# Kernel tuning notes

Measured on AMD Instinct MI355X. Metric: run time of the kernel, lower is better.

The kernel has to match this reference:

```python
import jax, jax.numpy as jnp
import numpy as np

N_EMB = 1024
N_HEADS = 16


def setup_inputs() -> dict:
    key = jax.random.key(0)
    k1, k2, k3 = jax.random.split(key, 3)
    x = jax.random.normal(k1, (2, 2048, N_EMB), dtype=jnp.float32)
    # qkv linear params (torch Linear: y = x @ W.T + b; store W as [in, 3*in])
    W_qkv = jax.random.normal(k2, (N_EMB, 3 * N_EMB), dtype=jnp.float32) * (1.0 / np.sqrt(N_EMB))
    b_qkv = jax.random.normal(k3, (3 * N_EMB,), dtype=jnp.float32) * 0.02
    return {"x": x, "W_qkv": W_qkv, "b_qkv": b_qkv}


def reference(x, W_qkv, b_qkv):
    B, S, D = x.shape
    H = N_HEADS
    Dh = D // H
    qkv = x @ W_qkv + b_qkv                       # [B, S, 3D]
    q, k, v = jnp.split(qkv, 3, axis=-1)
    # [B, S, D] -> [B, H, S, Dh]
    q = q.reshape(B, S, H, Dh).transpose(0, 2, 1, 3)
    k = k.reshape(B, S, H, Dh).transpose(0, 2, 1, 3)
    v = v.reshape(B, S, H, Dh).transpose(0, 2, 1, 3)
    scores = jnp.einsum("bhqd,bhkd->bhqk", q, k) * (1.0 / np.sqrt(Dh))
    attn = jax.nn.softmax(scores, axis=-1)        # no causal mask in original
    out = jnp.einsum("bhqk,bhkd->bhqd", attn, v)  # [B, H, S, Dh]
    return out.transpose(0, 2, 1, 3).reshape(B, S, D)
```

## Files before the change

### kernel.cpp

```cpp
#include <hip/hip_runtime.h>

#define S_LEN 2048
#define D_EMB 1024
#define H_CNT 16
#define DHD   64
#define N_QKV 3072

typedef __attribute__((ext_vector_type(8))) short short8;
typedef __attribute__((ext_vector_type(4))) float f32x4;
typedef __attribute__((ext_vector_type(4))) unsigned u32x4;
typedef unsigned short u16;

__device__ __forceinline__ u16 f2bf(float f) {
  unsigned u = __float_as_uint(f);
  u += 0x7FFFu + ((u >> 16) & 1u);
  return (u16)(u >> 16);
}

__device__ __forceinline__ unsigned cvtpk(float lo, float hi) {
  unsigned r;
  asm("v_cvt_pk_bf16_f32 %0, %1, %2" : "=v"(r) : "v"(lo), "v"(hi));
  return r;
}

__device__ __forceinline__ void gload16(const void* g, void* lds) {
  __builtin_amdgcn_global_load_lds(
      (const __attribute__((address_space(1))) void*)g,
      (__attribute__((address_space(3))) void*)lds, 16, 0, 0);
}

__global__ __launch_bounds__(256) void cvt_x_kern(const float* __restrict__ x,
                                                  u16* __restrict__ xb) {
  int i = blockIdx.x * 256 + threadIdx.x;
  float4 v = ((const float4*)x)[i];
  unsigned* o = (unsigned*)&((ushort4*)xb)[i];
  o[0] = cvtpk(v.x, v.y);
  o[1] = cvtpk(v.z, v.w);
}

__global__ __launch_bounds__(256) void cvt_wt_kern(const float* __restrict__ w,
                                                   u16* __restrict__ wt) {
  __shared__ u16 tile[64][65];
  const int ct = blockIdx.x, kt = blockIdx.y, t = threadIdx.x;
#pragma unroll
  for (int i = 0; i < 4; ++i) {
    int idx = t + i * 256;
    int kk = idx >> 4, c4 = (idx & 15) * 4;
    float4 v = *(const float4*)(w + (size_t)(kt * 64 + kk) * N_QKV + ct * 64 + c4);
    tile[kk][c4 + 0] = f2bf(v.x);
    tile[kk][c4 + 1] = f2bf(v.y);
    tile[kk][c4 + 2] = f2bf(v.z);
    tile[kk][c4 + 3] = f2bf(v.w);
  }
  __syncthreads();
#pragma unroll
  for (int i = 0; i < 2; ++i) {
    int id = t + i * 256;
    int c = id >> 3, k8 = (id & 7) * 8;
    short8 o;
#pragma unroll
    for (int j = 0; j < 8; ++j) o[j] = (short)tile[k8 + j][c];
    *(short8*)&wt[(size_t)(ct * 64 + c) * D_EMB + kt * 64 + k8] = o;
  }
}

__global__ __launch_bounds__(256) void qkv_gemm_kern(
    const u16* __restrict__ xb, const u16* __restrict__ wt,
    const float* __restrict__ bias,
    u16* __restrict__ qo, u16* __restrict__ ko, u16* __restrict__ vo) {
  __shared__ __align__(16) u16 SM[128 * 128];
  u16* As = SM;
  u16* Bs = SM + 128 * 64;
  const int t = threadIdx.x;
  const int w = t >> 6, l = t & 63, lr = l & 15, lg = l >> 4;
  const int wr = w >> 1, wc = w & 1;
  const int row0 = blockIdx.x * 128, col0 = blockIdx.y * 128;
  const int srow = l >> 3, scol = (l & 7) * 16;
  const int tsel = col0 >> 10;
  const bool ctq = (tsel < 2);

  f32x4 acc[4][4];
#pragma unroll
  for (int m = 0; m < 4; ++m)
#pragma unroll
    for (int n = 0; n < 4; ++n) acc[m][n] = (f32x4){0.f, 0.f, 0.f, 0.f};

  const int ldrow = w * 32;
  for (int ki = 0; ki < 16; ++ki) {
    int k0 = ki * 64;
#pragma unroll
    for (int c = 0; c < 4; ++c) {
      int tr = ldrow + c * 8 + srow;
      int sc = scol ^ ((tr & 7) << 4);
      gload16((const char*)xb + (size_t)(row0 + tr) * (D_EMB * 2) + k0 * 2 + sc,
              (char*)As + (ldrow + c * 8) * 128);
      gload16((const char*)wt + (size_t)(col0 + tr) * (D_EMB * 2) + k0 * 2 + sc,
              (char*)Bs + (ldrow + c * 8) * 128);
    }
    __syncthreads();
    const u16* Ab = ctq ? Bs : As;
    const u16* Bb = ctq ? As : Bs;
    const int ar0 = ctq ? wc * 64 : wr * 64;
    const int br0 = ctq ? wr * 64 : wc * 64;
    short8 bfr[4][2];
#pragma unroll
    for (int n = 0; n < 4; ++n) {
      int br = br0 + n * 16 + lr;
#pragma unroll
      for (int kk = 0; kk < 2; ++kk)
        bfr[n][kk] = *(const short8*)&Bb[(br << 6) + ((kk * 32 + lg * 8) ^ ((br & 7) << 3))];
    }
#pragma unroll
    for (int m = 0; m < 4; ++m) {
      int ar = ar0 + m * 16 + lr;
      short8 a0 = *(const short8*)&Ab[(ar << 6) + ((lg * 8) ^ ((ar & 7) << 3))];
      short8 a1 = *(const short8*)&Ab[(ar << 6) + ((32 + lg * 8) ^ ((ar & 7) << 3))];
#pragma unroll
      for (int n = 0; n < 4; ++n) {
        acc[m][n] = __builtin_amdgcn_mfma_f32_16x16x32_bf16(a0, bfr[n][0], acc[m][n], 0, 0, 0);
        acc[m][n] = __builtin_amdgcn_mfma_f32_16x16x32_bf16(a1, bfr[n][1], acc[m][n], 0, 0, 0);
      }
    }
    __syncthreads();
  }

  const int bb = row0 >> 11;
  if (ctq) {
    const float scl = (tsel == 0) ? (0.125f * 1.44269504f) : 1.0f;
    u16* dst = (tsel == 0) ? qo : ko;
#pragma unroll
    for (int m = 0; m < 4; ++m) {
      int qc0 = wc * 64 + m * 16 + lg * 4;
      float4 bn = *(const float4*)&bias[col0 + qc0];
#pragma unroll
      for (int n = 0; n < 4; ++n) {
        int s = wr * 64 + n * 16 + lr;
        uint2 pk;
        pk.x = cvtpk((acc[m][n][0] + bn.x) * scl, (acc[m][n][1] + bn.y) * scl);
        pk.y = cvtpk((acc[m][n][2] + bn.z) * scl, (acc[m][n][3] + bn.w) * scl);
        *(uint2*)&SM[(s << 7) + (qc0 ^ ((s & 7) << 3))] = pk;
      }
    }
    __syncthreads();
    const int c = t & 15, rl = t >> 4;
#pragma unroll
    for (int pass = 0; pass < 8; ++pass) {
      int s = pass * 16 + rl;
      short8 v = *(const short8*)&SM[(s << 7) + ((c ^ (s & 7)) << 3)];
      int d = (col0 + c * 8) & 1023, hh = d >> 6, dh = d & 63;
      *(short8*)(dst + ((size_t)(bb * H_CNT + hh) * S_LEN + (row0 & 2047) + s) * DHD + dh) = v;
    }
  } else {
#pragma unroll
    for (int n = 0; n < 4; ++n) {
      int qc = wc * 64 + n * 16 + lr;
      float bn = bias[col0 + qc];
#pragma unroll
      for (int m = 0; m < 4; ++m) {
        int s0l = wr * 64 + m * 16 + lg * 4;
        uint2 pk;
        pk.x = cvtpk(acc[m][n][0] + bn, acc[m][n][1] + bn);
        pk.y = cvtpk(acc[m][n][2] + bn, acc[m][n][3] + bn);
        *(uint2*)&SM[(qc << 7) + (s0l ^ ((qc & 7) << 3))] = pk;
      }
    }
    __syncthreads();
    const int c = t & 15, rl = t >> 4;
#pragma unroll
    for (int pass = 0; pass < 8; ++pass) {
      int qc = pass * 16 + rl;
      short8 v = *(const short8*)&SM[(qc << 7) + ((c ^ (qc & 7)) << 3)];
      int d = (col0 + qc) & 1023, hh = d >> 6, dh = d & 63;
      *(short8*)(vo + ((size_t)(bb * H_CNT + hh) * DHD + dh) * S_LEN +
                 (row0 & 2047) + c * 8) = v;
    }
  }
}

__global__ __launch_bounds__(256) void attn_kern(
    const u16* __restrict__ qp, const u16* __restrict__ kp,
    const u16* __restrict__ vtp, float* __restrict__ out) {
  __shared__ __align__(16) u16 Ks[2][64 * 64];
  __shared__ __align__(16) u16 Vs[2][64 * 64];
  const int t = threadIdx.x;
  const int w = t >> 6, l = t & 63, lr = l & 15, lg = l >> 4;
  const int qt = blockIdx.x, bh = blockIdx.y;
  const int b = bh >> 4, h = bh & 15;
  const int srow = l >> 3, scol = (l & 7) * 16;

  const u16* qbase = qp + ((size_t)bh * S_LEN + qt * 64 + w * 16) * DHD;
  short8 qf[2];
#pragma unroll
  for (int kk = 0; kk < 2; ++kk)
    qf[kk] = *(const short8*)(qbase + lr * DHD + kk * 32 + lg * 8);

  float mrun = -__builtin_inff(), lsum = 0.f;
  f32x4 oacc[4];
#pragma unroll
  for (int ct = 0; ct < 4; ++ct) oacc[ct] = (f32x4){0.f, 0.f, 0.f, 0.f};

  const int lbase0 = lr * 64 + ((lg * 8) ^ ((lr & 7) << 3));
  const int lbase1 = lr * 64 + ((32 + lg * 8) ^ ((lr & 7) << 3));
  const u16* kb00 = &Ks[0][lbase0];
  const u16* kb01 = &Ks[0][lbase1];
  const u16* kb10 = &Ks[1][lbase0];
  const u16* kb11 = &Ks[1][lbase1];
  const u16* vb00 = &Vs[0][lbase0];
  const u16* vb01 = &Vs[0][lbase1];
  const u16* vb10 = &Vs[1][lbase0];
  const u16* vb11 = &Vs[1][lbase1];

  int koff[2], voff[2];
#pragma unroll
  for (int c = 0; c < 2; ++c) {
    int row = w * 16 + c * 8 + srow;
    int sc = scol ^ ((row & 7) << 4);
    int tau = ((row & 15) >> 2) * 8 + ((row >> 4) & 1) * 4 + (row & 3) + (row >> 5) * 32;
    koff[c] = tau * 128 + sc;
    voff[c] = row * (S_LEN * 2) + sc;
  }
  const char* kpt = (const char*)(kp + (size_t)bh * S_LEN * DHD);
  const char* vpt = (const char*)(vtp + (size_t)bh * DHD * S_LEN);

#define ATTN_STAGE(BUF)                                                   \
  {                                                                       \
    _Pragma("unroll") for (int c = 0; c < 2; ++c) {                       \
      int r8 = w * 16 + c * 8;                                            \
      gload16(kpt + koff[c], (char*)Ks[BUF] + r8 * 128);                  \
      gload16(vpt + voff[c], (char*)Vs[BUF] + r8 * 128);                  \
    }                                                                     \
    kpt += 64 * 128;                                                      \
    vpt += 64 * 2;                                                        \
  }

#define ATTN_TILE(KB0, KB1, VB0, VB1, PF, PBUF)                                   \
  {                                                                               \
    if (PF) ATTN_STAGE(PBUF)                                                      \
    f32x4 st[4];                                                                  \
    _Pragma("unroll") for (int k2 = 0; k2 < 4; ++k2)                              \
        st[k2] = (f32x4){0.f, 0.f, 0.f, 0.f};                                     \
    __builtin_amdgcn_s_setprio(1);                                                \
    _Pragma("unroll") for (int k2 = 0; k2 < 4; ++k2) {                            \
      short8 a0 = *(const short8*)(KB0 + k2 * 1024);                              \
      short8 a1 = *(const short8*)(KB1 + k2 * 1024);                              \
      st[k2] = __builtin_amdgcn_mfma_f32_16x16x32_bf16(a0, qf[0], st[k2], 0, 0, 0); \
      st[k2] = __builtin_amdgcn_mfma_f32_16x16x32_bf16(a1, qf[1], st[k2], 0, 0, 0); \
    }                                                                             \
    __builtin_amdgcn_s_setprio(0);                                                \
    float mx = fmaxf(fmaxf(fmaxf(st[0][0], st[0][1]), fmaxf(st[0][2], st[0][3])), \
                     fmaxf(fmaxf(st[1][0], st[1][1]), fmaxf(st[1][2], st[1][3]))); \
    mx = fmaxf(mx, fmaxf(fmaxf(fmaxf(st[2][0], st[2][1]), fmaxf(st[2][2], st[2][3])), \
                         fmaxf(fmaxf(st[3][0], st[3][1]), fmaxf(st[3][2], st[3][3])))); \
    mx = fmaxf(mx, __shfl_xor(mx, 16, 64));                                       \
    mx = fmaxf(mx, __shfl_xor(mx, 32, 64));                                       \
    if (!__all(mx - mrun <= 8.0f)) {                                              \
      float mnew = fmaxf(mrun, mx);                                               \
      float fsc = exp2f(mrun - mnew);                                             \
      float fr[4];                                                                \
      _Pragma("unroll") for (int r = 0; r < 4; ++r)                               \
          fr[r] = __shfl(fsc, lg * 4 + r, 64);                                    \
      _Pragma("unroll") for (int ct = 0; ct < 4; ++ct)                            \
        _Pragma("unroll") for (int r = 0; r < 4; ++r) oacc[ct][r] *= fr[r];       \
      lsum *= fsc;                                                                \
      mrun = mnew;                                                                \
    }                                                                             \
    float rs = 0.f;                                                               \
    _Pragma("unroll") for (int k2 = 0; k2 < 4; ++k2)                              \
      _Pragma("unroll") for (int r = 0; r < 4; ++r) {                             \
        st[k2][r] = exp2f(st[k2][r] - mrun);                                      \
        rs += st[k2][r];                                                          \
      }                                                                           \
    rs += __shfl_xor(rs, 16, 64);                                                 \
    rs += __shfl_xor(rs, 32, 64);                                                 \
    lsum += rs;                                                                   \
    u32x4 ua, ub;                                                                 \
    ua[0] = cvtpk(st[0][0], st[0][1]); ua[1] = cvtpk(st[0][2], st[0][3]);         \
    ua[2] = cvtpk(st[1][0], st[1][1]); ua[3] = cvtpk(st[1][2], st[1][3]);         \
    ub[0] = cvtpk(st[2][0], st[2][1]); ub[1] = cvtpk(st[2][2], st[2][3]);         \
    ub[2] = cvtpk(st[3][0], st[3][1]); ub[3] = cvtpk(st[3][2], st[3][3]);         \
    short8 pa0 = __builtin_bit_cast(short8, ua);                                  \
    short8 pa1 = __builtin_bit_cast(short8, ub);                                  \
    __builtin_amdgcn_s_setprio(1);                                                \
    _Pragma("unroll") for (int ct = 0; ct < 4; ++ct) {                            \
      short8 bv0 = *(const short8*)(VB0 + ct * 1024);                             \
      short8 bv1 = *(const short8*)(VB1 + ct * 1024);                             \
      oacc[ct] = __builtin_amdgcn_mfma_f32_16x16x32_bf16(pa0, bv0, oacc[ct], 0, 0, 0); \
      oacc[ct] = __builtin_amdgcn_mfma_f32_16x16x32_bf16(pa1, bv1, oacc[ct], 0, 0, 0); \
    }                                                                             \
    __builtin_amdgcn_s_setprio(0);                                                \
    __syncthreads();                                                              \
  }

  ATTN_STAGE(0)
  __syncthreads();
  for (int ii = 0; ii < 16; ++ii) {
    ATTN_TILE(kb00, kb01, vb00, vb01, 1, 1)
    ATTN_TILE(kb10, kb11, vb10, vb11, ii < 15, 0)
  }

  float inv = 1.0f / lsum;
  float invr[4];
#pragma unroll
  for (int r = 0; r < 4; ++r) invr[r] = __shfl(inv, lg * 4 + r, 64);
  const int qg0 = qt * 64 + w * 16 + lg * 4;
#pragma unroll
  for (int ct = 0; ct < 4; ++ct) {
    int col = h * 64 + ct * 16 + lr;
#pragma unroll
    for (int r = 0; r < 4; ++r)
      out[((size_t)b * S_LEN + qg0 + r) * D_EMB + col] = oacc[ct][r] * invr[r];
  }
}

extern "C" void kernel_launch(void* const* d_in, const int* in_sizes, int n_in,
                              void* d_out, int out_size, void* d_ws, size_t ws_size,
                              hipStream_t stream) {
  (void)in_sizes; (void)n_in; (void)out_size; (void)ws_size;
  const float* x  = (const float*)d_in[0];
  const float* Wq = (const float*)d_in[1];
  const float* bq = (const float*)d_in[2];
  float* out = (float*)d_out;
  char* ws = (char*)d_ws;
  u16* xb = (u16*)(ws);
  u16* wt = (u16*)(ws + (size_t)8  * 1024 * 1024);
  u16* qb = (u16*)(ws + (size_t)14 * 1024 * 1024);
  u16* kb = (u16*)(ws + (size_t)22 * 1024 * 1024);
  u16* vb = (u16*)(ws + (size_t)30 * 1024 * 1024);

  cvt_x_kern <<<4096, 256, 0, stream>>>(x, xb);
  cvt_wt_kern<<<dim3(48, 16), 256, 0, stream>>>(Wq, wt);
  qkv_gemm_kern<<<dim3(32, 24), 256, 0, stream>>>(xb, wt, bq, qb, kb, vb);
  attn_kern  <<<dim3(32, 32), 256, 0, stream>>>(qb, kb, vb, out);
}
```

Before: 190.7 us.

## Process two 16-row query groups per wave in attention kernel

```diff
diff --git a/kernel.cpp b/kernel.cpp
--- a/kernel.cpp
+++ b/kernel.cpp
@@ -188,16 +188,21 @@
   const int b = bh >> 4, h = bh & 15;
   const int srow = l >> 3, scol = (l & 7) * 16;
 
-  const u16* qbase = qp + ((size_t)bh * S_LEN + qt * 64 + w * 16) * DHD;
-  short8 qf[2];
-#pragma unroll
-  for (int kk = 0; kk < 2; ++kk)
-    qf[kk] = *(const short8*)(qbase + lr * DHD + kk * 32 + lg * 8);
-
-  float mrun = -__builtin_inff(), lsum = 0.f;
-  f32x4 oacc[4];
-#pragma unroll
-  for (int ct = 0; ct < 4; ++ct) oacc[ct] = (f32x4){0.f, 0.f, 0.f, 0.f};
+  const u16* qbase = qp + ((size_t)bh * S_LEN + qt * 128 + w * 32) * DHD;
+  short8 qf00, qf01, qf10, qf11;
+  qf00 = *(const short8*)(qbase + lr * DHD + 0 * 32 + lg * 8);
+  qf01 = *(const short8*)(qbase + lr * DHD + 1 * 32 + lg * 8);
+  qf10 = *(const short8*)(qbase + (16 + lr) * DHD + 0 * 32 + lg * 8);
+  qf11 = *(const short8*)(qbase + (16 + lr) * DHD + 1 * 32 + lg * 8);
+
+  float mrun0 = -__builtin_inff(), lsum0 = 0.f;
+  float mrun1 = -__builtin_inff(), lsum1 = 0.f;
+  f32x4 oacc0[4], oacc1[4];
+#pragma unroll
+  for (int ct = 0; ct < 4; ++ct) {
+    oacc0[ct] = (f32x4){0.f, 0.f, 0.f, 0.f};
+    oacc1[ct] = (f32x4){0.f, 0.f, 0.f, 0.f};
+  }
 
   const int lbase0 = lr * 64 + ((lg * 8) ^ ((lr & 7) << 3));
   const int lbase1 = lr * 64 + ((32 + lg * 8) ^ ((lr & 7) << 3));
@@ -233,59 +238,72 @@
     vpt += 64 * 2;                                                        \
   }
 
+#define SOFTMAX_G(ST, MRUN, LSUM, OACC, PA0, PA1)                                 \
+  {                                                                               \
+    float mx = fmaxf(fmaxf(fmaxf(ST[0][0], ST[0][1]), fmaxf(ST[0][2], ST[0][3])), \
+                     fmaxf(fmaxf(ST[1][0], ST[1][1]), fmaxf(ST[1][2], ST[1][3]))); \
+    mx = fmaxf(mx, fmaxf(fmaxf(fmaxf(ST[2][0], ST[2][1]), fmaxf(ST[2][2], ST[2][3])), \
+                         fmaxf(fmaxf(ST[3][0], ST[3][1]), fmaxf(ST[3][2], ST[3][3])))); \
+    mx = fmaxf(mx, __shfl_xor(mx, 16, 64));                                       \
+    mx = fmaxf(mx, __shfl_xor(mx, 32, 64));                                       \
+    if (!__all(mx - MRUN <= 8.0f)) {                                              \
+      float mnew = fmaxf(MRUN, mx);                                               \
+      float fsc = exp2f(MRUN - mnew);                                             \
+      float fr[4];                                                                \
+      _Pragma("unroll") for (int r = 0; r < 4; ++r)                               \
+          fr[r] = __shfl(fsc, lg * 4 + r, 64);                                    \
+      _Pragma("unroll") for (int ct = 0; ct < 4; ++ct)                            \
+        _Pragma("unroll") for (int r = 0; r < 4; ++r) OACC[ct][r] *= fr[r];       \
+      LSUM *= fsc;                                                                \
+      MRUN = mnew;                                                                \
+    }                                                                             \
+    float rs = 0.f;                                                               \
+    _Pragma("unroll") for (int k2 = 0; k2 < 4; ++k2)                              \
+      _Pragma("unroll") for (int r = 0; r < 4; ++r) {                             \
+        ST[k2][r] = exp2f(ST[k2][r] - MRUN);                                      \
+        rs += ST[k2][r];                                                          \
+      }                                                                           \
+    rs += __shfl_xor(rs, 16, 64);                                                 \
+    rs += __shfl_xor(rs, 32, 64);                                                 \
+    LSUM += rs;                                                                   \
+    u32x4 ua, ub;                                                                 \
+    ua[0] = cvtpk(ST[0][0], ST[0][1]); ua[1] = cvtpk(ST[0][2], ST[0][3]);         \
+    ua[2] = cvtpk(ST[1][0], ST[1][1]); ua[3] = cvtpk(ST[1][2], ST[1][3]);         \
+    ub[0] = cvtpk(ST[2][0], ST[2][1]); ub[1] = cvtpk(ST[2][2], ST[2][3]);         \
+    ub[2] = cvtpk(ST[3][0], ST[3][1]); ub[3] = cvtpk(ST[3][2], ST[3][3]);         \
+    PA0 = __builtin_bit_cast(short8, ua);                                         \
+    PA1 = __builtin_bit_cast(short8, ub);                                         \
+  }
+
 #define ATTN_TILE(KB0, KB1, VB0, VB1, PF, PBUF)                                   \
   {                                                                               \
     if (PF) ATTN_STAGE(PBUF)                                                      \
-    f32x4 st[4];                                                                  \
-    _Pragma("unroll") for (int k2 = 0; k2 < 4; ++k2)                              \
-        st[k2] = (f32x4){0.f, 0.f, 0.f, 0.f};                                     \
+    f32x4 st0[4], st1[4];                                                         \
+    _Pragma("unroll") for (int k2 = 0; k2 < 4; ++k2) {                            \
+      st0[k2] = (f32x4){0.f, 0.f, 0.f, 0.f};                                      \
+      st1[k2] = (f32x4){0.f, 0.f, 0.f, 0.f};                                      \
+    }                                                                             \
     __builtin_amdgcn_s_setprio(1);                                                \
     _Pragma("unroll") for (int k2 = 0; k2 < 4; ++k2) {                            \
       short8 a0 = *(const short8*)(KB0 + k2 * 1024);                              \
       short8 a1 = *(const short8*)(KB1 + k2 * 1024);                              \
-      st[k2] = __builtin_amdgcn_mfma_f32_16x16x32_bf16(a0, qf[0], st[k2], 0, 0, 0); \
-      st[k2] = __builtin_amdgcn_mfma_f32_16x16x32_bf16(a1, qf[1], st[k2], 0, 0, 0); \
+      st0[k2] = __builtin_amdgcn_mfma_f32_16x16x32_bf16(a0, qf00, st0[k2], 0, 0, 0); \
+      st0[k2] = __builtin_amdgcn_mfma_f32_16x16x32_bf16(a1, qf01, st0[k2], 0, 0, 0); \
+      st1[k2] = __builtin_amdgcn_mfma_f32_16x16x32_bf16(a0, qf10, st1[k2], 0, 0, 0); \
+      st1[k2] = __builtin_amdgcn_mfma_f32_16x16x32_bf16(a1, qf11, st1[k2], 0, 0, 0); \
     }                                                                             \
     __builtin_amdgcn_s_setprio(0);                                                \
-    float mx = fmaxf(fmaxf(fmaxf(st[0][0], st[0][1]), fmaxf(st[0][2], st[0][3])), \
-                     fmaxf(fmaxf(st[1][0], st[1][1]), fmaxf(st[1][2], st[1][3]))); \
-    mx = fmaxf(mx, fmaxf(fmaxf(fmaxf(st[2][0], st[2][1]), fmaxf(st[2][2], st[2][3])), \
-                         fmaxf(fmaxf(st[3][0], st[3][1]), fmaxf(st[3][2], st[3][3])))); \
-    mx = fmaxf(mx, __shfl_xor(mx, 16, 64));                                       \
-    mx = fmaxf(mx, __shfl_xor(mx, 32, 64));                                       \
-    if (!__all(mx - mrun <= 8.0f)) {                                              \
-      float mnew = fmaxf(mrun, mx);                                               \
-      float fsc = exp2f(mrun - mnew);                                             \
-      float fr[4];                                                                \
-      _Pragma("unroll") for (int r = 0; r < 4; ++r)                               \
-          fr[r] = __shfl(fsc, lg * 4 + r, 64);                                    \
-      _Pragma("unroll") for (int ct = 0; ct < 4; ++ct)                            \
-        _Pragma("unroll") for (int r = 0; r < 4; ++r) oacc[ct][r] *= fr[r];       \
-      lsum *= fsc;                                                                \
-      mrun = mnew;                                                                \
-    }                                                                             \
-    float rs = 0.f;                                                               \
-    _Pragma("unroll") for (int k2 = 0; k2 < 4; ++k2)                              \
-      _Pragma("unroll") for (int r = 0; r < 4; ++r) {                             \
-        st[k2][r] = exp2f(st[k2][r] - mrun);                                      \
-        rs += st[k2][r];                                                          \
-      }                                                                           \
-    rs += __shfl_xor(rs, 16, 64);                                                 \
-    rs += __shfl_xor(rs, 32, 64);                                                 \
-    lsum += rs;                                                                   \
-    u32x4 ua, ub;                                                                 \
-    ua[0] = cvtpk(st[0][0], st[0][1]); ua[1] = cvtpk(st[0][2], st[0][3]);         \
-    ua[2] = cvtpk(st[1][0], st[1][1]); ua[3] = cvtpk(st[1][2], st[1][3]);         \
-    ub[0] = cvtpk(st[2][0], st[2][1]); ub[1] = cvtpk(st[2][2], st[2][3]);         \
-    ub[2] = cvtpk(st[3][0], st[3][1]); ub[3] = cvtpk(st[3][2], st[3][3]);         \
-    short8 pa0 = __builtin_bit_cast(short8, ua);                                  \
-    short8 pa1 = __builtin_bit_cast(short8, ub);                                  \
+    short8 pa00, pa01, pa10, pa11;                                                \
+    SOFTMAX_G(st0, mrun0, lsum0, oacc0, pa00, pa01)                               \
+    SOFTMAX_G(st1, mrun1, lsum1, oacc1, pa10, pa11)                               \
     __builtin_amdgcn_s_setprio(1);                                                \
     _Pragma("unroll") for (int ct = 0; ct < 4; ++ct) {                            \
       short8 bv0 = *(const short8*)(VB0 + ct * 1024);                             \
       short8 bv1 = *(const short8*)(VB1 + ct * 1024);                             \
-      oacc[ct] = __builtin_amdgcn_mfma_f32_16x16x32_bf16(pa0, bv0, oacc[ct], 0, 0, 0); \
-      oacc[ct] = __builtin_amdgcn_mfma_f32_16x16x32_bf16(pa1, bv1, oacc[ct], 0, 0, 0); \
+      oacc0[ct] = __builtin_amdgcn_mfma_f32_16x16x32_bf16(pa00, bv0, oacc0[ct], 0, 0, 0); \
+      oacc0[ct] = __builtin_amdgcn_mfma_f32_16x16x32_bf16(pa01, bv1, oacc0[ct], 0, 0, 0); \
+      oacc1[ct] = __builtin_amdgcn_mfma_f32_16x16x32_bf16(pa10, bv0, oacc1[ct], 0, 0, 0); \
+      oacc1[ct] = __builtin_amdgcn_mfma_f32_16x16x32_bf16(pa11, bv1, oacc1[ct], 0, 0, 0); \
     }                                                                             \
     __builtin_amdgcn_s_setprio(0);                                                \
     __syncthreads();                                                              \
@@ -298,17 +316,22 @@
     ATTN_TILE(kb10, kb11, vb10, vb11, ii < 15, 0)
   }
 
-  float inv = 1.0f / lsum;
-  float invr[4];
-#pragma unroll
-  for (int r = 0; r < 4; ++r) invr[r] = __shfl(inv, lg * 4 + r, 64);
-  const int qg0 = qt * 64 + w * 16 + lg * 4;
+  float inv0 = 1.0f / lsum0, inv1 = 1.0f / lsum1;
+  float invr0[4], invr1[4];
+#pragma unroll
+  for (int r = 0; r < 4; ++r) {
+    invr0[r] = __shfl(inv0, lg * 4 + r, 64);
+    invr1[r] = __shfl(inv1, lg * 4 + r, 64);
+  }
+  const int qg0 = qt * 128 + w * 32 + lg * 4;
 #pragma unroll
   for (int ct = 0; ct < 4; ++ct) {
     int col = h * 64 + ct * 16 + lr;
 #pragma unroll
-    for (int r = 0; r < 4; ++r)
-      out[((size_t)b * S_LEN + qg0 + r) * D_EMB + col] = oacc[ct][r] * invr[r];
+    for (int r = 0; r < 4; ++r) {
+      out[((size_t)b * S_LEN + qg0 + r) * D_EMB + col] = oacc0[ct][r] * invr0[r];
+      out[((size_t)b * S_LEN + qg0 + 16 + r) * D_EMB + col] = oacc1[ct][r] * invr1[r];
+    }
   }
 }
 
@@ -330,5 +353,5 @@
   cvt_x_kern <<<4096, 256, 0, stream>>>(x, xb);
   cvt_wt_kern<<<dim3(48, 16), 256, 0, stream>>>(Wq, wt);
   qkv_gemm_kern<<<dim3(32, 24), 256, 0, stream>>>(xb, wt, bq, qb, kb, vb);
-  attn_kern  <<<dim3(32, 32), 256, 0, stream>>>(qb, kb, vb, out);
-}
+  attn_kern  <<<dim3(16, 32), 256, 0, stream>>>(qb, kb, vb, out);
+}
```

Result: slower. 196.0 us (+2.8%).
